# Performance work log

Hardware: AMD Instinct MI355X
Metric: run time of the kernel (lower is better)

The kernel has to match this reference:

```python
import jax, jax.numpy as jnp
import numpy as np

B, N, F_IN, F_OUT = 8, 2048, 128, 128


def setup_inputs() -> dict:
    key = jax.random.key(0)
    k1, k2, k3, k4 = jax.random.split(key, 4)
    stdv = 1.0 / np.sqrt(F_OUT)
    X = jax.random.normal(k1, (B, N, F_IN), dtype=jnp.float32)
    adj = jax.random.uniform(k2, (B, N, N), dtype=jnp.float32)
    W = jax.random.uniform(k3, (F_IN, F_OUT), minval=-stdv, maxval=stdv, dtype=jnp.float32)
    b = jax.random.uniform(k4, (F_OUT,), minval=-stdv, maxval=stdv, dtype=jnp.float32)
    return {"X": X, "adj": adj, "W": W, "b": b}


def reference(X, adj, W, b):
    # XW: [B, N, F_out]
    XW = jnp.einsum('bnf,fo->bno', X, W)
    # adj + I (self loops)
    adj = adj + jnp.eye(adj.shape[1], dtype=adj.dtype)[None]
    # symmetric degree normalization: D^-1/2 A D^-1/2, done as row/col scaling
    d = jnp.sum(adj, axis=-1)                 # [B, N]
    r = d ** -0.5                             # [B, N]
    adj = adj * r[:, :, None] * r[:, None, :] # [B, N, N]
    y = jnp.einsum('bnm,bmo->bno', adj, XW) + b
    return jax.nn.leaky_relu(y, negative_slope=0.01)
```

## Files before the change

kernel.cpp:

```cpp
#include <hip/hip_runtime.h>
#include <hip/hip_bf16.h>

#define BB 8
#define NN 2048
#define FD 128

typedef float f32x4 __attribute__((ext_vector_type(4)));
typedef short bf16x8 __attribute__((ext_vector_type(8)));
typedef short s16x4 __attribute__((ext_vector_type(4)));

__device__ __forceinline__ short f2bf(float f) {
  union { __hip_bfloat16 h; short s; } u;
  u.h = __float2bfloat16(f);
  return u.s;
}

__global__ __launch_bounds__(256) void k_degree(const float* __restrict__ adj,
                                                float* __restrict__ r) {
  const int row  = blockIdx.x * 4 + (threadIdx.x >> 6);
  const int lane = threadIdx.x & 63;
  const f32x4* p = reinterpret_cast<const f32x4*>(adj + (size_t)row * NN);
  float s = 0.f;
#pragma unroll
  for (int i = 0; i < 8; ++i) {
    f32x4 v = p[lane + 64 * i];
    s += (v.x + v.y) + (v.z + v.w);
  }
#pragma unroll
  for (int off = 32; off >= 1; off >>= 1) s += __shfl_xor(s, off, 64);
  if (lane == 0) r[row] = rsqrtf(1.0f + s);
}

__global__ __launch_bounds__(256) void k_xw(const float* __restrict__ X,
                                            const float* __restrict__ W,
                                            const float* __restrict__ r,
                                            short* __restrict__ bpack,
                                            float* __restrict__ xwsr) {
  __shared__ __align__(16) float Xs[64][132];
  __shared__ __align__(16) float Ws[128][128];
  const int b  = blockIdx.y;
  const int m0 = blockIdx.x * 64;
  const int t  = threadIdx.x;
  {
    const f32x4* wp = reinterpret_cast<const f32x4*>(W);
    f32x4* wd = reinterpret_cast<f32x4*>(&Ws[0][0]);
#pragma unroll
    for (int i = 0; i < 16; ++i) wd[t + 256 * i] = wp[t + 256 * i];
    const f32x4* xp = reinterpret_cast<const f32x4*>(X + ((size_t)b * NN + m0) * FD);
#pragma unroll
    for (int i = 0; i < 8; ++i) {
      int slot = t + 256 * i;
      f32x4 v = xp[slot];
      *reinterpret_cast<f32x4*>(&Xs[slot >> 5][(slot & 31) * 4]) = v;
    }
  }
  __syncthreads();
  const int ot = (t & 15) * 8;
  const int mt = (t >> 4) * 4;
  float acc[4][8];
#pragma unroll
  for (int i = 0; i < 4; ++i)
#pragma unroll
    for (int j = 0; j < 8; ++j) acc[i][j] = 0.f;

  for (int k = 0; k < 128; k += 4) {
    f32x4 xv[4];
#pragma unroll
    for (int i = 0; i < 4; ++i) xv[i] = *reinterpret_cast<const f32x4*>(&Xs[mt + i][k]);
#pragma unroll
    for (int kk = 0; kk < 4; ++kk) {
      float wv[8];
#pragma unroll
      for (int j = 0; j < 8; ++j) wv[j] = Ws[k + kk][ot + j];
#pragma unroll
      for (int i = 0; i < 4; ++i)
#pragma unroll
        for (int j = 0; j < 8; ++j) acc[i][j] = fmaf(xv[i][kk], wv[j], acc[i][j]);
    }
  }
  const int bm = b * NN + m0 + mt;
#pragma unroll
  for (int i = 0; i < 4; ++i) {
    float rm = r[bm + i];
#pragma unroll
    for (int j = 0; j < 8; ++j) acc[i][j] *= rm;
  }
#pragma unroll
  for (int i = 0; i < 4; ++i) {
    f32x4 lo = {acc[i][0], acc[i][1], acc[i][2], acc[i][3]};
    f32x4 hi = {acc[i][4], acc[i][5], acc[i][6], acc[i][7]};
    float* dst = xwsr + (size_t)(bm + i) * FD + ot;
    *reinterpret_cast<f32x4*>(dst) = lo;
    *reinterpret_cast<f32x4*>(dst + 4) = hi;
  }
  short* bp = bpack + (size_t)b * NN * FD;
  const int grp = (m0 + mt) >> 3;
  const int h   = ((m0 + mt) >> 2) & 1;
#pragma unroll
  for (int j = 0; j < 8; ++j) {
    s16x4 sv;
#pragma unroll
    for (int i = 0; i < 4; ++i) sv[i] = f2bf(acc[i][j]);
    *reinterpret_cast<s16x4*>(bp + (size_t)grp * 1024 + (ot + j) * 8 + h * 4) = sv;
  }
}

__global__ __launch_bounds__(256) void k_gemm2(const float* __restrict__ adj,
                                               const short* __restrict__ bpack,
                                               const float* __restrict__ xwsr,
                                               const float* __restrict__ r,
                                               const float* __restrict__ bias,
                                               float* __restrict__ out) {
  __shared__ float Red[2][16][132];
  const int b     = blockIdx.y;
  const int n0    = blockIdx.x * 32;
  const int t     = threadIdx.x;
  const int lane  = t & 63;
  const int w     = t >> 6;
  const int strip = w & 1;
  const int khalf = w >> 1;
  const int rowb  = n0 + strip * 16;

  const float* ap  = adj + ((size_t)b * NN + rowb + (lane & 15)) * NN + khalf * 1024 + (lane >> 4) * 8;
  const short* bpb = bpack + (size_t)b * NN * FD + (size_t)(khalf * 128 + (lane >> 4)) * 1024 + (lane & 15) * 8;

  f32x4 acc[8];
#pragma unroll
  for (int i = 0; i < 8; ++i) acc[i] = (f32x4){0.f, 0.f, 0.f, 0.f};

  f32x4 aS[4][2];
  bf16x8 bS[2][8];

  auto loadA = [&](int ks, f32x4 (&d)[2]) {
    const f32x4* q = reinterpret_cast<const f32x4*>(ap + ks * 32);
    d[0] = q[0];
    d[1] = q[1];
  };
  auto loadB = [&](int ks, bf16x8 (&d)[8]) {
    const short* p = bpb + (size_t)ks * 4096;
#pragma unroll
    for (int ct = 0; ct < 8; ++ct)
      d[ct] = *reinterpret_cast<const bf16x8*>(p + ct * 128);
  };
  auto step = [&](f32x4 (&sa)[2], bf16x8 (&sb)[8]) {
    bf16x8 af;
#pragma unroll
    for (int i = 0; i < 4; ++i) { af[i] = f2bf(sa[0][i]); af[4 + i] = f2bf(sa[1][i]); }
    __builtin_amdgcn_s_setprio(1);
#pragma unroll
    for (int ct = 0; ct < 8; ++ct)
      acc[ct] = __builtin_amdgcn_mfma_f32_16x16x32_bf16(af, sb[ct], acc[ct], 0, 0, 0);
    __builtin_amdgcn_s_setprio(0);
  };

  loadA(0, aS[0]); loadA(1, aS[1]); loadA(2, aS[2]); loadA(3, aS[3]);
  loadB(0, bS[0]); loadB(1, bS[1]);
#pragma unroll
  for (int ks = 0; ks < 32; ++ks) {
    step(aS[ks & 3], bS[ks & 1]);
    if (ks + 4 < 32) loadA(ks + 4, aS[ks & 3]);
    if (ks + 2 < 32) loadB(ks + 2, bS[ks & 1]);
  }

  const int col = lane & 15, rq = lane >> 4;
  if (khalf == 1) {
#pragma unroll
    for (int reg = 0; reg < 4; ++reg)
#pragma unroll
      for (int ct = 0; ct < 8; ++ct)
        Red[strip][rq * 4 + reg][ct * 16 + col] = acc[ct][reg];
  }
  __syncthreads();
  if (khalf == 0) {
    const float* xr = xwsr + ((size_t)b * NN + rowb) * FD;
    float* ob = out + ((size_t)b * NN + rowb) * FD;
#pragma unroll
    for (int reg = 0; reg < 4; ++reg) {
      const int rloc = rq * 4 + reg;
      const float rn = r[b * NN + rowb + rloc];
#pragma unroll
      for (int ct = 0; ct < 8; ++ct) {
        const int o = ct * 16 + col;
        float v = acc[ct][reg] + Red[strip][rloc][o] + xr[(size_t)rloc * FD + o];
        v = rn * v + bias[o];
        ob[(size_t)rloc * FD + o] = v > 0.f ? v : 0.01f * v;
      }
    }
  }
}

extern "C" void kernel_launch(void* const* d_in, const int* in_sizes, int n_in,
                              void* d_out, int out_size, void* d_ws, size_t ws_size,
                              hipStream_t stream) {
  (void)in_sizes; (void)n_in; (void)out_size; (void)ws_size;
  const float* X    = (const float*)d_in[0];
  const float* adj  = (const float*)d_in[1];
  const float* W    = (const float*)d_in[2];
  const float* bias = (const float*)d_in[3];
  float* out = (float*)d_out;

  char* ws = (char*)d_ws;
  float* r     = (float*)ws;
  short* bpack = (short*)(ws + 65536);
  float* xwsr  = (float*)(ws + 4259840);

  k_degree<<<dim3(BB * NN / 4), dim3(256), 0, stream>>>(adj, r);
  k_xw<<<dim3(NN / 64, BB), dim3(256), 0, stream>>>(X, W, r, bpack, xwsr);
  k_gemm2<<<dim3(NN / 32, BB), dim3(256), 0, stream>>>(adj, bpack, xwsr, r, bias, out);
}
```

Baseline: 75.27 us.

## Split output columns across waves instead of splitting K with LDS reduction

The adj-times-XW kernel now gives each block 16 rows, and each of its four waves owns 32 output columns over the full K range. This replaces the previous split-K scheme, which used two row strips and two K halves joined by an LDS reduction and a barrier. The new layout removes the shared-memory reduction and the sync, launches twice as many blocks, and sets a launch bound of 4 for occupancy. In exchange, all four waves now load the same adj rows, so adj traffic per block is redundant and depends on cache hits. Each wave also issues fewer MFMAs per A load.

```diff
diff --git a/kernel.cpp b/kernel.cpp
--- a/kernel.cpp
+++ b/kernel.cpp
@@ -105,86 +105,71 @@
   }
 }
 
-__global__ __launch_bounds__(256) void k_gemm2(const float* __restrict__ adj,
-                                               const short* __restrict__ bpack,
-                                               const float* __restrict__ xwsr,
-                                               const float* __restrict__ r,
-                                               const float* __restrict__ bias,
-                                               float* __restrict__ out) {
-  __shared__ float Red[2][16][132];
-  const int b     = blockIdx.y;
-  const int n0    = blockIdx.x * 32;
-  const int t     = threadIdx.x;
-  const int lane  = t & 63;
-  const int w     = t >> 6;
-  const int strip = w & 1;
-  const int khalf = w >> 1;
-  const int rowb  = n0 + strip * 16;
+__global__ __launch_bounds__(256, 4) void k_gemm4(const float* __restrict__ adj,
+                                                  const short* __restrict__ bpack,
+                                                  const float* __restrict__ xwsr,
+                                                  const float* __restrict__ r,
+                                                  const float* __restrict__ bias,
+                                                  float* __restrict__ out) {
+  const int b    = blockIdx.y;
+  const int n0   = blockIdx.x * 16;
+  const int t    = threadIdx.x;
+  const int lane = t & 63;
+  const int w    = t >> 6;
 
-  const float* ap  = adj + ((size_t)b * NN + rowb + (lane & 15)) * NN + khalf * 1024 + (lane >> 4) * 8;
-  const short* bpb = bpack + (size_t)b * NN * FD + (size_t)(khalf * 128 + (lane >> 4)) * 1024 + (lane & 15) * 8;
+  const float* ap  = adj + ((size_t)b * NN + n0 + (lane & 15)) * NN + (lane >> 4) * 8;
+  const short* bpb = bpack + (size_t)b * NN * FD + (size_t)(lane >> 4) * 1024
+                   + (w * 32 + (lane & 15)) * 8;
 
-  f32x4 acc[8];
-#pragma unroll
-  for (int i = 0; i < 8; ++i) acc[i] = (f32x4){0.f, 0.f, 0.f, 0.f};
+  f32x4 acc[2];
+  acc[0] = (f32x4){0.f, 0.f, 0.f, 0.f};
+  acc[1] = (f32x4){0.f, 0.f, 0.f, 0.f};
 
-  f32x4 aS[4][2];
-  bf16x8 bS[2][8];
+  f32x4  aS[4][2];
+  bf16x8 bS[4][2];
 
   auto loadA = [&](int ks, f32x4 (&d)[2]) {
     const f32x4* q = reinterpret_cast<const f32x4*>(ap + ks * 32);
     d[0] = q[0];
     d[1] = q[1];
   };
-  auto loadB = [&](int ks, bf16x8 (&d)[8]) {
+  auto loadB = [&](int ks, bf16x8 (&d)[2]) {
     const short* p = bpb + (size_t)ks * 4096;
-#pragma unroll
-    for (int ct = 0; ct < 8; ++ct)
-      d[ct] = *reinterpret_cast<const bf16x8*>(p + ct * 128);
+    d[0] = *reinterpret_cast<const bf16x8*>(p);
+    d[1] = *reinterpret_cast<const bf16x8*>(p + 128);
   };
-  auto step = [&](f32x4 (&sa)[2], bf16x8 (&sb)[8]) {
+  auto step = [&](f32x4 (&sa)[2], bf16x8 (&sb)[2]) {
     bf16x8 af;
 #pragma unroll
     for (int i = 0; i < 4; ++i) { af[i] = f2bf(sa[0][i]); af[4 + i] = f2bf(sa[1][i]); }
-    __builtin_amdgcn_s_setprio(1);
-#pragma unroll
-    for (int ct = 0; ct < 8; ++ct)
-      acc[ct] = __builtin_amdgcn_mfma_f32_16x16x32_bf16(af, sb[ct], acc[ct], 0, 0, 0);
-    __builtin_amdgcn_s_setprio(0);
+    acc[0] = __builtin_amdgcn_mfma_f32_16x16x32_bf16(af, sb[0], acc[0], 0, 0, 0);
+    acc[1] = __builtin_amdgcn_mfma_f32_16x16x32_bf16(af, sb[1], acc[1], 0, 0, 0);
   };
 
-  loadA(0, aS[0]); loadA(1, aS[1]); loadA(2, aS[2]); loadA(3, aS[3]);
-  loadB(0, bS[0]); loadB(1, bS[1]);
 #pragma unroll
-  for (int ks = 0; ks < 32; ++ks) {
-    step(aS[ks & 3], bS[ks & 1]);
-    if (ks + 4 < 32) loadA(ks + 4, aS[ks & 3]);
-    if (ks + 2 < 32) loadB(ks + 2, bS[ks & 1]);
+  for (int i = 0; i < 4; ++i) { loadA(i, aS[i]); loadB(i, bS[i]); }
+#pragma unroll 4
+  for (int ks = 0; ks < 60; ++ks) {
+    step(aS[ks & 3], bS[ks & 3]);
+    loadA(ks + 4, aS[ks & 3]);
+    loadB(ks + 4, bS[ks & 3]);
   }
+#pragma unroll
+  for (int ks = 60; ks < 64; ++ks) step(aS[ks & 3], bS[ks & 3]);
 
   const int col = lane & 15, rq = lane >> 4;
-  if (khalf == 1) {
+  const float* xr = xwsr + ((size_t)b * NN + n0) * FD;
+  float* ob = out + ((size_t)b * NN + n0) * FD;
 #pragma unroll
-    for (int reg = 0; reg < 4; ++reg)
+  for (int reg = 0; reg < 4; ++reg) {
+    const int rloc = rq * 4 + reg;
+    const float rn = r[b * NN + n0 + rloc];
 #pragma unroll
-      for (int ct = 0; ct < 8; ++ct)
-        Red[strip][rq * 4 + reg][ct * 16 + col] = acc[ct][reg];
-  }
-  __syncthreads();
-  if (khalf == 0) {
-    const float* xr = xwsr + ((size_t)b * NN + rowb) * FD;
-    float* ob = out + ((size_t)b * NN + rowb) * FD;
-#pragma unroll
-    for (int reg = 0; reg < 4; ++reg) {
-      const int rloc = rq * 4 + reg;
-      const float rn = r[b * NN + rowb + rloc];
-#pragma unroll
-      for (int ct = 0; ct < 8; ++ct) {
-        const int o = ct * 16 + col;
-        float v = acc[ct][reg] + Red[strip][rloc][o] + xr[(size_t)rloc * FD + o];
-        v = rn * v + bias[o];
-        ob[(size_t)rloc * FD + o] = v > 0.f ? v : 0.01f * v;
-      }
+    for (int ct = 0; ct < 2; ++ct) {
+      const int o = w * 32 + ct * 16 + col;
+      float v = acc[ct][reg] + xr[(size_t)rloc * FD + o];
+      v = rn * v + bias[o];
+      ob[(size_t)rloc * FD + o] = v > 0.f ? v : 0.01f * v;
     }
   }
 }
@@ -206,5 +191,5 @@
 
   k_degree<<<dim3(BB * NN / 4), dim3(256), 0, stream>>>(adj, r);
   k_xw<<<dim3(NN / 64, BB), dim3(256), 0, stream>>>(X, W, r, bpack, xwsr);
-  k_gemm2<<<dim3(NN / 32, BB), dim3(256), 0, stream>>>(adj, bpack, xwsr, r, bias, out);
+  k_gemm4<<<dim3(NN / 16, BB), dim3(256), 0, stream>>>(adj, bpack, xwsr, r, bias, out);
 }
```

Result: slower. 114.9 us (+52.6%).
